# Performance work log

Hardware: AMD Instinct MI355X
Metric: run time of the kernel (lower is better)

Reference implementation:

```python
import jax, jax.numpy as jnp
import numpy as np

H = 128        # hidden_channels
R = 32         # num_rbf
L = 2          # num_layers
CUTOFF = 4.5   # cutoff_upper (cutoff_lower = 0)
N_ATOMS = 2048
N_EDGES = 32768


def _tensor_norm(t):
    # Frobenius norm squared over the trailing 3x3 -> [N, H]
    return jnp.sum(t * t, axis=(-2, -1))


def _decompose(t):
    # Split into isotropic (I), antisymmetric (A), traceless symmetric (S) parts.
    eye = jnp.eye(3, dtype=t.dtype)
    I = (jnp.trace(t, axis1=-2, axis2=-1) / 3.0)[..., None, None] * eye
    A = 0.5 * (t - jnp.swapaxes(t, -2, -1))
    S = 0.5 * (t + jnp.swapaxes(t, -2, -1)) - I
    return I, A, S


def _chan_mix(T, W):
    # torch nn.Linear(H, H, bias=False) applied on the channel axis of [N,H,3,3]
    return jnp.einsum('nhij,gh->ngij', T, W)


def _interaction(X, edge_index, edge_weight, edge_attr, q,
                 W1, b1, W2, b2, W3, b3, Wt):
    N = X.shape[0]
    src, dst = edge_index[0], edge_index[1]
    # cosine cutoff (cutoff_lower = 0)
    C = 0.5 * (jnp.cos(edge_weight * (jnp.pi / CUTOFF)) + 1.0)
    C = C * (edge_weight < CUTOFF).astype(C.dtype)
    # edge scalar MLP: R -> H -> 2H -> 3H, silu
    ea = jax.nn.silu(edge_attr @ W1.T + b1)
    ea = jax.nn.silu(ea @ W2.T + b2)
    ea = jax.nn.silu(ea @ W3.T + b3)
    ea = (ea * C[:, None]).reshape(-1, H, 3)       # [E, H, 3]
    # normalize node tensors
    X = X / (_tensor_norm(X) + 1.0)[..., None, None]
    I, A, S = _decompose(X)
    I = _chan_mix(I, Wt[0])
    A = _chan_mix(A, Wt[1])
    S = _chan_mix(S, Wt[2])
    Y = I + A + S
    # per-edge tensor messages (Im + Am + Sm fused before the scatter)
    msg = (ea[:, :, 0, None, None] * I[dst]
           + ea[:, :, 1, None, None] * A[dst]
           + ea[:, :, 2, None, None] * S[dst])   # [E, H, 3, 3]
    M = jax.ops.segment_sum(msg, src, num_segments=N)
    # O(3) group: symmetrized tensor product, scaled by charge factor
    AB = jnp.matmul(M, Y) + jnp.matmul(Y, M)
    I, A, S = _decompose((1.0 + 0.1 * q[:, None, None, None]) * AB)
    normp1 = (_tensor_norm(I + A + S) + 1.0)[..., None, None]
    I, A, S = I / normp1, A / normp1, S / normp1
    I = _chan_mix(I, Wt[3])
    A = _chan_mix(A, Wt[4])
    S = _chan_mix(S, Wt[5])
    dX = I + A + S
    return X + dX + (1.0 + 0.1 * q[:, None, None, None]) * jnp.matmul(dX, dX)


def setup_inputs() -> dict:
    key = jax.random.key(0)
    ks = jax.random.split(key, 10)
    N, E = N_ATOMS, N_EDGES
    X = jax.random.normal(ks[0], (N, H, 3, 3), jnp.float32)
    edge_index = jax.random.randint(ks[1], (2, E), 0, N, jnp.int32)
    edge_weight = jax.random.uniform(ks[2], (E,), jnp.float32, 0.1, CUTOFF)
    edge_attr = jax.random.normal(ks[3], (E, R), jnp.float32)
    q = jax.random.normal(ks[4], (N,), jnp.float32) * 0.1
    s = 0.05
    Ws1 = jax.random.normal(ks[5], (L, H, R), jnp.float32) * s
    bs1 = jnp.zeros((L, H), jnp.float32)
    Ws2 = jax.random.normal(ks[6], (L, 2 * H, H), jnp.float32) * s
    bs2 = jnp.zeros((L, 2 * H), jnp.float32)
    Ws3 = jax.random.normal(ks[7], (L, 3 * H, 2 * H), jnp.float32) * s
    bs3 = jnp.zeros((L, 3 * H), jnp.float32)
    Wt = jax.random.normal(ks[8], (L, 6, H, H), jnp.float32) * s
    return dict(X=X, edge_attr=edge_attr, edge_weight=edge_weight, q=q,
                Ws1=Ws1, bs1=bs1, Ws2=Ws2, bs2=bs2, Ws3=Ws3, bs3=bs3,
                Wt=Wt, edge_index=edge_index)


def reference(X, edge_attr, edge_weight, q, Ws1, bs1, Ws2, bs2, Ws3, bs3, Wt, edge_index):
    for l in range(L):
        X = _interaction(X, edge_index, edge_weight, edge_attr, q,
                         Ws1[l], bs1[l], Ws2[l], bs2[l], Ws3[l], bs3[l], Wt[l])
    return X
```

## Files before the change

### kernel.cpp

```cpp
#include <hip/hip_runtime.h>
#include <hip/hip_bf16.h>
#include <math.h>

#define H 128
#define R 32
#define NATOMS 2048
#define NEDGES 32768
#define NH (NATOMS * H)
#define NP 1152
#define CUTOFF_F 4.5f
#define PI_OVER_CUTOFF 0.6981317007977318f

typedef __bf16 bf16x8 __attribute__((ext_vector_type(8)));
typedef float f32x4 __attribute__((ext_vector_type(4)));
typedef short short8 __attribute__((ext_vector_type(8)));

__device__ __forceinline__ float silu_f(float x) {
    return x / (1.f + __expf(-x));
}
__device__ __forceinline__ float b2f(unsigned short u) {
    return __uint_as_float(((unsigned)u) << 16);
}
__device__ __forceinline__ unsigned short f2b(float f) {
    __hip_bfloat16 h = __float2bfloat16(f);
    return __builtin_bit_cast(unsigned short, h);
}

__device__ __forceinline__ void build_full(const float d[9], float m[9]) {
    float i0 = d[0], a01 = d[1], a02 = d[2], a12 = d[3];
    float s00 = d[4], s01 = d[5], s02 = d[6], s11 = d[7], s12 = d[8];
    float s22 = -(s00 + s11);
    m[0] = i0 + s00;  m[1] = a01 + s01;  m[2] = a02 + s02;
    m[3] = s01 - a01; m[4] = i0 + s11;   m[5] = a12 + s12;
    m[6] = s02 - a02; m[7] = s12 - a12;  m[8] = i0 + s22;
}

#define C0 (NEDGES * R)
#define C1 (2 * H * R)
#define C2 (2 * 2 * H * H)
#define C3 (2 * 3 * H * 2 * H)
#define C4 (2 * 6 * H * H)
__global__ __launch_bounds__(256) void k_cast_all(
        const float* __restrict__ ea, const float* __restrict__ w1,
        const float* __restrict__ w2, const float* __restrict__ w3,
        const float* __restrict__ wt,
        __hip_bfloat16* __restrict__ oea, __hip_bfloat16* __restrict__ ow1,
        __hip_bfloat16* __restrict__ ow2, __hip_bfloat16* __restrict__ ow3,
        __hip_bfloat16* __restrict__ owt) {
    int i = blockIdx.x * 256 + threadIdx.x;
    if (i < C0) { oea[i] = __float2bfloat16(ea[i]); return; }
    i -= C0;
    if (i < C1) { ow1[i] = __float2bfloat16(w1[i]); return; }
    i -= C1;
    if (i < C2) { ow2[i] = __float2bfloat16(w2[i]); return; }
    i -= C2;
    if (i < C3) { ow3[i] = __float2bfloat16(w3[i]); return; }
    i -= C3;
    if (i < C4) { owt[i] = __float2bfloat16(wt[i]); }
}

__global__ __launch_bounds__(256) void k_node_prep(
        const float* __restrict__ X, float* __restrict__ Xn,
        __hip_bfloat16* __restrict__ Db) {
    int i = blockIdx.x * 256 + threadIdx.x;
    if (i >= NH) return;
    const float* x = X + (size_t)i * 9;
    float v[9];
    float ss = 0.f;
#pragma unroll
    for (int j = 0; j < 9; j++) { v[j] = x[j]; ss += v[j] * v[j]; }
    float inv = 1.f / (ss + 1.f);
#pragma unroll
    for (int j = 0; j < 9; j++) { v[j] *= inv; Xn[(size_t)i * 9 + j] = v[j]; }
    float i0 = (v[0] + v[4] + v[8]) * (1.f / 3.f);
    unsigned short* D = (unsigned short*)Db + (size_t)(i >> 7) * NP + (i & 127);
    D[0 * H] = f2b(i0);
    D[1 * H] = f2b(0.5f * (v[1] - v[3]));
    D[2 * H] = f2b(0.5f * (v[2] - v[6]));
    D[3 * H] = f2b(0.5f * (v[5] - v[7]));
    D[4 * H] = f2b(v[0] - i0);
    D[5 * H] = f2b(0.5f * (v[1] + v[3]));
    D[6 * H] = f2b(0.5f * (v[2] + v[6]));
    D[7 * H] = f2b(v[4] - i0);
    D[8 * H] = f2b(0.5f * (v[5] + v[7]));
}

struct TGm {
    static constexpr int BKm = 64;
    static constexpr int RB  = 128;
    static constexpr int SWZ = 7;
    static constexpr int NIT = 2;
    static constexpr int ABYTES = 128 * RB;
    static constexpr int BBYTES = 64 * RB;
    static constexpr int AISS = ABYTES / 4096;
    static constexpr int BISS = BBYTES / 4096;
    static constexpr int LDSB = ABYTES + BBYTES;
};

__device__ __forceinline__ void tile_gemm_mix(
        const __hip_bfloat16* __restrict__ A, int strideA,
        const __hip_bfloat16* __restrict__ W,
        int m0, int n0, char* lds, f32x4 acc[4][2]) {
    using T = TGm;
    const int t = threadIdx.x;
    const int lane = t & 63;
    const int w = t >> 6;

    auto stage = [&](int b, int it) {
        const int k0 = it * T::BKm;
        char* As = lds + b * T::LDSB;
        char* Bs = As + T::ABYTES;
#pragma unroll
        for (int i = 0; i < T::AISS; i++) {
            int base = (w * T::AISS + i) * 1024;
            int lin = base + lane * 16;
            int row = lin / T::RB;
            int slot = (lin % T::RB) >> 4;
            int sl = slot ^ (row & T::SWZ);
            const char* src = (const char*)(A + (size_t)(m0 + row) * strideA + k0) + sl * 16;
            __builtin_amdgcn_global_load_lds(
                (const __attribute__((address_space(1))) void*)src,
                (__attribute__((address_space(3))) void*)(As + base), 16, 0, 0);
        }
#pragma unroll
        for (int i = 0; i < T::BISS; i++) {
            int base = (w * T::BISS + i) * 1024;
            int lin = base + lane * 16;
            int row = lin / T::RB;
            int slot = (lin % T::RB) >> 4;
            int sl = slot ^ (row & T::SWZ);
            const char* src = (const char*)(W + (size_t)(n0 + row) * H + k0) + sl * 16;
            __builtin_amdgcn_global_load_lds(
                (const __attribute__((address_space(1))) void*)src,
                (__attribute__((address_space(3))) void*)(Bs + base), 16, 0, 0);
        }
    };

    auto compute = [&](int b) {
        const char* As = lds + b * T::LDSB;
        const char* Bs = As + T::ABYTES;
        const int wm = (w & 1) * 64;
        const int wn = (w >> 1) * 32;
        const int rA = wm + (lane & 15);
        const int rB = wn + (lane & 15);
        const int c = lane >> 4;
#pragma unroll
        for (int kk = 0; kk < T::BKm / 32; kk++) {
            bf16x8 av[4], bv[2];
#pragma unroll
            for (int mf = 0; mf < 4; mf++) {
                int row = rA + mf * 16;
                int sp = (kk * 4 + c) ^ (row & T::SWZ);
                av[mf] = __builtin_bit_cast(bf16x8,
                    *(const short8*)(As + row * T::RB + sp * 16));
            }
#pragma unroll
            for (int nf = 0; nf < 2; nf++) {
                int row = rB + nf * 16;
                int sp = (kk * 4 + c) ^ (row & T::SWZ);
                bv[nf] = __builtin_bit_cast(bf16x8,
                    *(const short8*)(Bs + row * T::RB + sp * 16));
            }
#pragma unroll
            for (int mf = 0; mf < 4; mf++)
#pragma unroll
                for (int nf = 0; nf < 2; nf++)
                    acc[mf][nf] = __builtin_amdgcn_mfma_f32_16x16x32_bf16(
                        av[mf], bv[nf], acc[mf][nf], 0, 0, 0);
        }
    };

    stage(0, 0);
    asm volatile("s_waitcnt vmcnt(0)" ::: "memory");
    __syncthreads();
    for (int it = 0; it < T::NIT; it++) {
        int b = it & 1;
        if (it + 1 < T::NIT) stage(b ^ 1, it + 1);
        compute(b);
        asm volatile("s_waitcnt vmcnt(0)" ::: "memory");
        __syncthreads();
    }
}

__global__ __launch_bounds__(256) void k_mix(
        const __hip_bfloat16* __restrict__ Db, const __hip_bfloat16* __restrict__ Wtb,
        __hip_bfloat16* __restrict__ Outp, int partOff) {
    __shared__ char lds[2 * TGm::LDSB];
    int c = blockIdx.z;
    int part = (c == 0) ? 0 : ((c < 4) ? 1 : 2);
    const __hip_bfloat16* A = Db + (size_t)c * H;
    const __hip_bfloat16* W = Wtb + (size_t)(partOff + part) * H * H;
    unsigned short* Out = (unsigned short*)Outp + (size_t)c * H;
    const int lane = threadIdx.x & 63;
    const int w = threadIdx.x >> 6;
    const int wm = (w & 1) * 64, wn = (w >> 1) * 32;
    const int m0 = blockIdx.x * 128, n0 = blockIdx.y * 64;
    f32x4 acc[4][2] = {};
    tile_gemm_mix(A, NP, W, m0, n0, lds, acc);
#pragma unroll
    for (int mf = 0; mf < 4; mf++)
#pragma unroll
        for (int r = 0; r < 4; r++) {
            int row = m0 + wm + mf * 16 + (lane >> 4) * 4 + r;
#pragma unroll
            for (int nf = 0; nf < 2; nf++) {
                int col = n0 + wn + nf * 16 + (lane & 15);
                Out[(size_t)row * NP + col] = f2b(acc[mf][nf][r]);
            }
        }
}

#define ETILE 64
#define PAD0 40
#define PAD1 136
#define PAD2 264
#define SA2_B (64 * PAD2 * 2)
#define SA1_B (64 * PAD1 * 2)

__global__ __launch_bounds__(256, 3) void k_mlp_fused(
        const __hip_bfloat16* __restrict__ eaB,
        const __hip_bfloat16* __restrict__ W1b, const __hip_bfloat16* __restrict__ W2b,
        const __hip_bfloat16* __restrict__ W3b,
        const float* __restrict__ bs1, const float* __restrict__ bs2,
        const float* __restrict__ bs3, const float* __restrict__ ew,
        __hip_bfloat16* __restrict__ ea3g) {
    const int l = blockIdx.z;
    const unsigned short* W1 = (const unsigned short*)W1b + (size_t)l * (H * R);
    const unsigned short* W2 = (const unsigned short*)W2b + (size_t)l * (2 * H * H);
    const unsigned short* W3 = (const unsigned short*)W3b + (size_t)l * (3 * H * 2 * H);
    const float* b1 = bs1 + (size_t)l * H;
    const float* b2 = bs2 + (size_t)l * 2 * H;
    const float* b3 = bs3 + (size_t)l * 3 * H;
    unsigned short* outp = (unsigned short*)ea3g + (size_t)l * NEDGES * 384;
    const int e0 = blockIdx.x * ETILE;

    __shared__ char smem[SA2_B + SA1_B + 256 + 16];
    unsigned short* sA2 = (unsigned short*)smem;
    unsigned short* sEA = (unsigned short*)smem;
    unsigned short* sA1 = (unsigned short*)(smem + SA2_B);
    float* sEW = (float*)(smem + SA2_B + SA1_B);

    const int t = threadIdx.x;
    const int lane = t & 63;
    const int w = t >> 6;
    const int q = lane >> 4;
    const int li = lane & 15;

    {
        int row = t >> 2, c8 = t & 3;
        *(uint4*)(sEA + row * PAD0 + c8 * 8) =
            *(const uint4*)((const unsigned short*)eaB + (size_t)(e0 + row) * R + c8 * 8);
        if (t < ETILE) sEW[t] = ew[e0 + t];
    }
    __syncthreads();

    {
        f32x4 acc1[4][2] = {};
        bf16x8 bv[2];
#pragma unroll
        for (int nf = 0; nf < 2; nf++) {
            int col = w * 32 + nf * 16 + li;
            bv[nf] = __builtin_bit_cast(bf16x8,
                *(const short8*)(W1 + (size_t)col * R + q * 8));
        }
#pragma unroll
        for (int mf = 0; mf < 4; mf++) {
            int row = mf * 16 + li;
            bf16x8 av = __builtin_bit_cast(bf16x8,
                *(const short8*)(sEA + row * PAD0 + q * 8));
#pragma unroll
            for (int nf = 0; nf < 2; nf++)
                acc1[mf][nf] = __builtin_amdgcn_mfma_f32_16x16x32_bf16(
                    av, bv[nf], acc1[mf][nf], 0, 0, 0);
        }
        float bb[2];
#pragma unroll
        for (int nf = 0; nf < 2; nf++) bb[nf] = b1[w * 32 + nf * 16 + li];
        __syncthreads();
#pragma unroll
        for (int mf = 0; mf < 4; mf++)
#pragma unroll
            for (int r = 0; r < 4; r++) {
                int row = mf * 16 + q * 4 + r;
#pragma unroll
                for (int nf = 0; nf < 2; nf++) {
                    int col = w * 32 + nf * 16 + li;
                    sA1[row * PAD1 + col] = f2b(silu_f(acc1[mf][nf][r] + bb[nf]));
                }
            }
    }
    __syncthreads();

    {
        f32x4 acc2[4][4] = {};
        bf16x8 b2v[2][4];
#pragma unroll
        for (int nf = 0; nf < 4; nf++)
            b2v[0][nf] = __builtin_bit_cast(bf16x8,
                *(const short8*)(W2 + (size_t)(w * 64 + nf * 16 + li) * H + q * 8));
#pragma unroll
        for (int ks = 0; ks < 4; ks++) {
            const int cur = ks & 1;
            if (ks < 3) {
#pragma unroll
                for (int nf = 0; nf < 4; nf++)
                    b2v[cur ^ 1][nf] = __builtin_bit_cast(bf16x8,
                        *(const short8*)(W2 + (size_t)(w * 64 + nf * 16 + li) * H
                                         + (ks + 1) * 32 + q * 8));
            }
            bf16x8 av[4];
#pragma unroll
            for (int mf = 0; mf < 4; mf++)
                av[mf] = __builtin_bit_cast(bf16x8,
                    *(const short8*)(sA1 + (mf * 16 + li) * PAD1 + ks * 32 + q * 8));
            __builtin_amdgcn_s_setprio(1);
#pragma unroll
            for (int mf = 0; mf < 4; mf++)
#pragma unroll
                for (int nf = 0; nf < 4; nf++)
                    acc2[mf][nf] = __builtin_amdgcn_mfma_f32_16x16x32_bf16(
                        av[mf], b2v[cur][nf], acc2[mf][nf], 0, 0, 0);
            __builtin_amdgcn_s_setprio(0);
        }
        float bb[4];
#pragma unroll
        for (int nf = 0; nf < 4; nf++) bb[nf] = b2[w * 64 + nf * 16 + li];
        __syncthreads();
#pragma unroll
        for (int mf = 0; mf < 4; mf++)
#pragma unroll
            for (int r = 0; r < 4; r++) {
                int row = mf * 16 + q * 4 + r;
#pragma unroll
                for (int nf = 0; nf < 4; nf++) {
                    int col = w * 64 + nf * 16 + li;
                    sA2[row * PAD2 + col] = f2b(silu_f(acc2[mf][nf][r] + bb[nf]));
                }
            }
    }
    __syncthreads();

#pragma unroll
    for (int hn = 0; hn < 2; hn++) {
        const int cbase = w * 96 + hn * 48;
        f32x4 acc3[4][3] = {};
        bf16x8 b3v[2][3];
#pragma unroll
        for (int nf = 0; nf < 3; nf++)
            b3v[0][nf] = __builtin_bit_cast(bf16x8,
                *(const short8*)(W3 + (size_t)(cbase + nf * 16 + li) * (2 * H) + q * 8));
#pragma unroll
        for (int ks = 0; ks < 8; ks++) {
            const int cur = ks & 1;
            if (ks < 7) {
#pragma unroll
                for (int nf = 0; nf < 3; nf++)
                    b3v[cur ^ 1][nf] = __builtin_bit_cast(bf16x8,
                        *(const short8*)(W3 + (size_t)(cbase + nf * 16 + li) * (2 * H)
                                         + (ks + 1) * 32 + q * 8));
            }
            bf16x8 av[4];
#pragma unroll
            for (int mf = 0; mf < 4; mf++)
                av[mf] = __builtin_bit_cast(bf16x8,
                    *(const short8*)(sA2 + (mf * 16 + li) * PAD2 + ks * 32 + q * 8));
            __builtin_amdgcn_s_setprio(1);
#pragma unroll
            for (int mf = 0; mf < 4; mf++)
#pragma unroll
                for (int nf = 0; nf < 3; nf++)
                    acc3[mf][nf] = __builtin_amdgcn_mfma_f32_16x16x32_bf16(
                        av[mf], b3v[cur][nf], acc3[mf][nf], 0, 0, 0);
            __builtin_amdgcn_s_setprio(0);
        }
        float bb[3];
#pragma unroll
        for (int nf = 0; nf < 3; nf++) bb[nf] = b3[cbase + nf * 16 + li];
#pragma unroll
        for (int mf = 0; mf < 4; mf++)
#pragma unroll
            for (int r = 0; r < 4; r++) {
                int row = mf * 16 + q * 4 + r;
                float wv = sEW[row];
                float cs = (wv < CUTOFF_F) ? 0.5f * (__cosf(wv * PI_OVER_CUTOFF) + 1.f) : 0.f;
#pragma unroll
                for (int nf = 0; nf < 3; nf++) {
                    int col = cbase + nf * 16 + li;
                    float x = silu_f(acc3[mf][nf][r] + bb[nf]) * cs;
                    outp[(size_t)(e0 + row) * 384 + col] = f2b(x);
                }
            }
    }
}

__global__ __launch_bounds__(256) void k_hist(
        const int* __restrict__ eidx, int* __restrict__ cnt) {
    int e = blockIdx.x * 256 + threadIdx.x;
    if (e < NEDGES) atomicAdd(&cnt[eidx[e]], 1);
}

__global__ __launch_bounds__(256) void k_scan(
        const int* __restrict__ cnt, int* __restrict__ rowstart,
        int* __restrict__ cursor) {
    __shared__ int partial[256];
    int t = threadIdx.x;
    int loc[8];
    int run = 0;
#pragma unroll
    for (int j = 0; j < 8; j++) {
        int v = cnt[t * 8 + j];
        loc[j] = run; run += v;
    }
    partial[t] = run;
    __syncthreads();
    if (t == 0) {
        int acc = 0;
        for (int i = 0; i < 256; i++) { int v = partial[i]; partial[i] = acc; acc += v; }
        rowstart[2048] = acc;
    }
    __syncthreads();
    int base = partial[t];
#pragma unroll
    for (int j = 0; j < 8; j++) {
        rowstart[t * 8 + j] = base + loc[j];
        cursor[t * 8 + j] = base + loc[j];
    }
}

__global__ __launch_bounds__(256) void k_fill(
        const int* __restrict__ eidx, int* __restrict__ cursor,
        int* __restrict__ elist) {
    int e = blockIdx.x * 256 + threadIdx.x;
    if (e >= NEDGES) return;
    int src = eidx[e];
    int pos = atomicAdd(&cursor[src], 1);
    elist[pos] = e;
}

__global__ __launch_bounds__(256) void k_gather_ab(
        const __hip_bfloat16* __restrict__ ea ,
        const int* __restrict__ eidx,
        const int* __restrict__ rowstart, const int* __restrict__ elist,
        const __hip_bfloat16* __restrict__ Yb, const float* __restrict__ q,
        __hip_bfloat16* __restrict__ Tb) {
    int gid = blockIdx.x * 256 + threadIdx.x;
    int n = gid >> 7;
    int t7 = gid & 127;
    int hp = t7 >> 1;
    int half = t7 & 1;
    int h0 = hp << 1;
    int beg = rowstart[n], end = rowstart[n + 1];
    const unsigned short* Y = (const unsigned short*)Yb;
    float acc[9][2];
#pragma unroll
    for (int c = 0; c < 9; c++) { acc[c][0] = 0.f; acc[c][1] = 0.f; }
    for (int idx = beg + half; idx < end; idx += 2) {
        int e = elist[idx];
        int dst = eidx[NEDGES + e];
        const unsigned short* eap = (const unsigned short*)ea + (size_t)e * 384 + h0 * 3;
        unsigned u0 = *(const unsigned*)(eap);
        unsigned u1 = *(const unsigned*)(eap + 2);
        unsigned u2 = *(const unsigned*)(eap + 4);
        float w0a = b2f(u0 & 0xffff), w1a = b2f(u0 >> 16);
        float w2a = b2f(u1 & 0xffff), w0b = b2f(u1 >> 16);
        float w1b = b2f(u2 & 0xffff), w2b = b2f(u2 >> 16);
        const unsigned short* yp = Y + (size_t)dst * NP + h0;
        ushort2 y;
        y = *(const ushort2*)(yp + 0 * H); acc[0][0] += w0a * b2f(y.x); acc[0][1] += w0b * b2f(y.y);
        y = *(const ushort2*)(yp + 1 * H); acc[1][0] += w1a * b2f(y.x); acc[1][1] += w1b * b2f(y.y);
        y = *(const ushort2*)(yp + 2 * H); acc[2][0] += w1a * b2f(y.x); acc[2][1] += w1b * b2f(y.y);
        y = *(const ushort2*)(yp + 3 * H); acc[3][0] += w1a * b2f(y.x); acc[3][1] += w1b * b2f(y.y);
#pragma unroll
        for (int c = 4; c < 9; c++) {
            y = *(const ushort2*)(yp + c * H);
            acc[c][0] += w2a * b2f(y.x); acc[c][1] += w2b * b2f(y.y);
        }
    }
#pragma unroll
    for (int c = 0; c < 9; c++) {
        acc[c][0] += __shfl_xor(acc[c][0], 1);
        acc[c][1] += __shfl_xor(acc[c][1], 1);
    }
    int hcol = h0 + half;
    const unsigned short* yp = Y + (size_t)n * NP + hcol;
    float scale = 1.f + 0.1f * q[n];
    float md[9], yd[9];
#pragma unroll
    for (int c = 0; c < 9; c++) {
        md[c] = acc[c][half];
        yd[c] = b2f(yp[(size_t)c * H]);
    }
    float m[9], yf[9];
    build_full(md, m);
    build_full(yd, yf);
    float ab[9];
#pragma unroll
    for (int ii = 0; ii < 3; ii++)
#pragma unroll
        for (int jj = 0; jj < 3; jj++) {
            float s = 0.f;
#pragma unroll
            for (int kk = 0; kk < 3; kk++)
                s += m[ii * 3 + kk] * yf[kk * 3 + jj] + yf[ii * 3 + kk] * m[kk * 3 + jj];
            ab[ii * 3 + jj] = s;
        }
    float nrm = 0.f;
#pragma unroll
    for (int j = 0; j < 9; j++) { ab[j] *= scale; nrm += ab[j] * ab[j]; }
    float inv = 1.f / (nrm + 1.f);
    float tr3 = (ab[0] + ab[4] + ab[8]) * (1.f / 3.f);
    unsigned short* T = (unsigned short*)Tb + (size_t)n * NP + hcol;
    T[0 * H] = f2b(tr3 * inv);
    T[1 * H] = f2b(0.5f * (ab[1] - ab[3]) * inv);
    T[2 * H] = f2b(0.5f * (ab[2] - ab[6]) * inv);
    T[3 * H] = f2b(0.5f * (ab[5] - ab[7]) * inv);
    T[4 * H] = f2b((ab[0] - tr3) * inv);
    T[5 * H] = f2b(0.5f * (ab[1] + ab[3]) * inv);
    T[6 * H] = f2b(0.5f * (ab[2] + ab[6]) * inv);
    T[7 * H] = f2b((ab[4] - tr3) * inv);
    T[8 * H] = f2b(0.5f * (ab[5] + ab[7]) * inv);
}

template <bool PREP>
__global__ __launch_bounds__(256) void k_final(
        const __hip_bfloat16* __restrict__ dXb, const float* __restrict__ Xn,
        const float* __restrict__ q, float* __restrict__ Xout,
        float* __restrict__ XnW, __hip_bfloat16* __restrict__ Db) {
    int i = blockIdx.x * 256 + threadIdx.x;
    if (i >= NH) return;
    const unsigned short* dX = (const unsigned short*)dXb + (size_t)(i >> 7) * NP + (i & 127);
    float dd[9];
#pragma unroll
    for (int c = 0; c < 9; c++) dd[c] = b2f(dX[(size_t)c * H]);
    float dx[9];
    build_full(dd, dx);
    float scale = 1.f + 0.1f * q[i >> 7];
    float out[9];
#pragma unroll
    for (int ii = 0; ii < 3; ii++)
#pragma unroll
        for (int jj = 0; jj < 3; jj++) {
            float s = 0.f;
#pragma unroll
            for (int kk = 0; kk < 3; kk++)
                s += dx[ii * 3 + kk] * dx[kk * 3 + jj];
            out[ii * 3 + jj] = Xn[(size_t)i * 9 + ii * 3 + jj] + dx[ii * 3 + jj] + scale * s;
        }
#pragma unroll
    for (int j = 0; j < 9; j++) Xout[(size_t)i * 9 + j] = out[j];
    if (PREP) {
        float ss = 0.f;
#pragma unroll
        for (int j = 0; j < 9; j++) ss += out[j] * out[j];
        float inv = 1.f / (ss + 1.f);
        float v[9];
#pragma unroll
        for (int j = 0; j < 9; j++) { v[j] = out[j] * inv; XnW[(size_t)i * 9 + j] = v[j]; }
        float i0 = (v[0] + v[4] + v[8]) * (1.f / 3.f);
        unsigned short* D = (unsigned short*)Db + (size_t)(i >> 7) * NP + (i & 127);
        D[0 * H] = f2b(i0);
        D[1 * H] = f2b(0.5f * (v[1] - v[3]));
        D[2 * H] = f2b(0.5f * (v[2] - v[6]));
        D[3 * H] = f2b(0.5f * (v[5] - v[7]));
        D[4 * H] = f2b(v[0] - i0);
        D[5 * H] = f2b(0.5f * (v[1] + v[3]));
        D[6 * H] = f2b(0.5f * (v[2] + v[6]));
        D[7 * H] = f2b(v[4] - i0);
        D[8 * H] = f2b(0.5f * (v[5] + v[7]));
    }
}

extern "C" void kernel_launch(void* const* d_in, const int* in_sizes, int n_in,
                              void* d_out, int out_size, void* d_ws, size_t ws_size,
                              hipStream_t stream) {
    const float* X          = (const float*)d_in[0];
    const float* edge_attr  = (const float*)d_in[1];
    const float* edge_weight= (const float*)d_in[2];
    const float* q          = (const float*)d_in[3];
    const float* Ws1        = (const float*)d_in[4];
    const float* bs1        = (const float*)d_in[5];
    const float* Ws2        = (const float*)d_in[6];
    const float* bs2        = (const float*)d_in[7];
    const float* Ws3        = (const float*)d_in[8];
    const float* bs3        = (const float*)d_in[9];
    const float* Wt         = (const float*)d_in[10];
    const int*   eidx       = (const int*)d_in[11];
    float* Xout = (float*)d_out;

    char* p = (char*)d_ws;
    auto alloc = [&](size_t bytes) -> char* {
        char* r = p; p += (bytes + 255) & ~(size_t)255; return r;
    };
    size_t nodeBytes = (size_t)NH * 9 * sizeof(float);
    float* Xn   = (float*)alloc(nodeBytes);
    __hip_bfloat16* Db = (__hip_bfloat16*)alloc((size_t)NH * 9 * 2);
    __hip_bfloat16* Yb = (__hip_bfloat16*)alloc((size_t)NH * 9 * 2);
    __hip_bfloat16* eaB = (__hip_bfloat16*)alloc((size_t)C0 * 2);
    __hip_bfloat16* W1b = (__hip_bfloat16*)alloc((size_t)C1 * 2);
    __hip_bfloat16* W2b = (__hip_bfloat16*)alloc((size_t)C2 * 2);
    __hip_bfloat16* W3b = (__hip_bfloat16*)alloc((size_t)C3 * 2);
    __hip_bfloat16* Wtb = (__hip_bfloat16*)alloc((size_t)C4 * 2);
    __hip_bfloat16* ea3g = (__hip_bfloat16*)alloc((size_t)2 * NEDGES * 384 * 2);
    int* cnt      = (int*)alloc(2048 * 4);
    int* rowstart = (int*)alloc(2049 * 4);
    int* cursor   = (int*)alloc(2048 * 4);
    int* elist    = (int*)alloc(NEDGES * 4);

    k_cast_all<<<(C0 + C1 + C2 + C3 + C4) / 256, 256, 0, stream>>>(
        edge_attr, Ws1, Ws2, Ws3, Wt, eaB, W1b, W2b, W3b, Wtb);

    hipMemsetAsync(cnt, 0, 2048 * sizeof(int), stream);
    k_hist<<<NEDGES / 256, 256, 0, stream>>>(eidx, cnt);
    k_scan<<<1, 256, 0, stream>>>(cnt, rowstart, cursor);
    k_fill<<<NEDGES / 256, 256, 0, stream>>>(eidx, cursor, elist);

    k_node_prep<<<NH / 256, 256, 0, stream>>>(X, Xn, Db);

    k_mlp_fused<<<dim3(NEDGES / ETILE, 1, 2), 256, 0, stream>>>(
        eaB, W1b, W2b, W3b, bs1, bs2, bs3, edge_weight, ea3g);

    for (int l = 0; l < 2; l++) {
        const __hip_bfloat16* Wtl = Wtb + (size_t)l * 6 * H * H;
        const __hip_bfloat16* ea3 = ea3g + (size_t)l * NEDGES * 384;

        k_mix<<<dim3(NATOMS / 128, 2, 9), 256, 0, stream>>>(Db, Wtl, Yb, 0);
        k_gather_ab<<<NH / 256, 256, 0, stream>>>(
            ea3, eidx, rowstart, elist, Yb, q, Db);
        k_mix<<<dim3(NATOMS / 128, 2, 9), 256, 0, stream>>>(Db, Wtl, Yb, 3);
        if (l == 0)
            k_final<true><<<NH / 256, 256, 0, stream>>>(Yb, Xn, q, Xout, Xn, Db);
        else
            k_final<false><<<NH / 256, 256, 0, stream>>>(Yb, Xn, q, Xout, nullptr, nullptr);
    }
}
```

Before: 166.4 us.

## Split fused edge MLP across 8 waves per block instead of 4

The fused edge MLP kernel now launches 512 threads per block and divides each layer's output columns among 8 wavefronts, so each wave handles half as many MFMA column fragments. This is meant to raise wave-level parallelism and latency hiding per block and to cut the per-wave accumulator register footprint. In exchange, each weight fragment is loaded by more waves and the final stage is split unevenly into 2+1 fragments per wave. Occupancy limits also change with the new launch bounds.

```diff
diff --git a/kernel.cpp b/kernel.cpp
--- a/kernel.cpp
+++ b/kernel.cpp
@@ -214,10 +214,10 @@
 #define PAD0 40
 #define PAD1 136
 #define PAD2 264
-#define SA2_B (64 * PAD2 * 2)
-#define SA1_B (64 * PAD1 * 2)
-
-__global__ __launch_bounds__(256, 3) void k_mlp_fused(
+#define SA2_B (ETILE * PAD2 * 2)
+#define SA1_B (ETILE * PAD1 * 2)
+
+__global__ __launch_bounds__(512, 4) void k_mlp_fused(
         const __hip_bfloat16* __restrict__ eaB,
         const __hip_bfloat16* __restrict__ W1b, const __hip_bfloat16* __restrict__ W2b,
         const __hip_bfloat16* __restrict__ W3b,
@@ -234,7 +234,7 @@
     unsigned short* outp = (unsigned short*)ea3g + (size_t)l * NEDGES * 384;
     const int e0 = blockIdx.x * ETILE;
 
-    __shared__ char smem[SA2_B + SA1_B + 256 + 16];
+    __shared__ char smem[SA2_B + SA1_B + ETILE * 4 + 16];
     unsigned short* sA2 = (unsigned short*)smem;
     unsigned short* sEA = (unsigned short*)smem;
     unsigned short* sA1 = (unsigned short*)(smem + SA2_B);
@@ -247,65 +247,55 @@
     const int li = lane & 15;
 
     {
-        int row = t >> 2, c8 = t & 3;
-        *(uint4*)(sEA + row * PAD0 + c8 * 8) =
-            *(const uint4*)((const unsigned short*)eaB + (size_t)(e0 + row) * R + c8 * 8);
+        if (t < 256) {
+            int row = t >> 2, c8 = t & 3;
+            *(uint4*)(sEA + row * PAD0 + c8 * 8) =
+                *(const uint4*)((const unsigned short*)eaB + (size_t)(e0 + row) * R + c8 * 8);
+        }
         if (t < ETILE) sEW[t] = ew[e0 + t];
     }
     __syncthreads();
 
     {
-        f32x4 acc1[4][2] = {};
-        bf16x8 bv[2];
-#pragma unroll
-        for (int nf = 0; nf < 2; nf++) {
-            int col = w * 32 + nf * 16 + li;
-            bv[nf] = __builtin_bit_cast(bf16x8,
-                *(const short8*)(W1 + (size_t)col * R + q * 8));
-        }
+        f32x4 acc1[4] = {};
+        const int col = w * 16 + li;
+        bf16x8 bv = __builtin_bit_cast(bf16x8,
+            *(const short8*)(W1 + (size_t)col * R + q * 8));
 #pragma unroll
         for (int mf = 0; mf < 4; mf++) {
             int row = mf * 16 + li;
             bf16x8 av = __builtin_bit_cast(bf16x8,
                 *(const short8*)(sEA + row * PAD0 + q * 8));
-#pragma unroll
-            for (int nf = 0; nf < 2; nf++)
-                acc1[mf][nf] = __builtin_amdgcn_mfma_f32_16x16x32_bf16(
-                    av, bv[nf], acc1[mf][nf], 0, 0, 0);
-        }
-        float bb[2];
-#pragma unroll
-        for (int nf = 0; nf < 2; nf++) bb[nf] = b1[w * 32 + nf * 16 + li];
+            acc1[mf] = __builtin_amdgcn_mfma_f32_16x16x32_bf16(
+                av, bv, acc1[mf], 0, 0, 0);
+        }
+        float bb = b1[col];
         __syncthreads();
 #pragma unroll
         for (int mf = 0; mf < 4; mf++)
 #pragma unroll
             for (int r = 0; r < 4; r++) {
                 int row = mf * 16 + q * 4 + r;
-#pragma unroll
-                for (int nf = 0; nf < 2; nf++) {
-                    int col = w * 32 + nf * 16 + li;
-                    sA1[row * PAD1 + col] = f2b(silu_f(acc1[mf][nf][r] + bb[nf]));
-                }
+                sA1[row * PAD1 + col] = f2b(silu_f(acc1[mf][r] + bb));
             }
     }
     __syncthreads();
 
     {
-        f32x4 acc2[4][4] = {};
-        bf16x8 b2v[2][4];
-#pragma unroll
-        for (int nf = 0; nf < 4; nf++)
+        f32x4 acc2[4][2] = {};
+        bf16x8 b2v[2][2];
+#pragma unroll
+        for (int nf = 0; nf < 2; nf++)
             b2v[0][nf] = __builtin_bit_cast(bf16x8,
-                *(const short8*)(W2 + (size_t)(w * 64 + nf * 16 + li) * H + q * 8));
+                *(const short8*)(W2 + (size_t)(w * 32 + nf * 16 + li) * H + q * 8));
 #pragma unroll
         for (int ks = 0; ks < 4; ks++) {
             const int cur = ks & 1;
             if (ks < 3) {
 #pragma unroll
-                for (int nf = 0; nf < 4; nf++)
+                for (int nf = 0; nf < 2; nf++)
                     b2v[cur ^ 1][nf] = __builtin_bit_cast(bf16x8,
-                        *(const short8*)(W2 + (size_t)(w * 64 + nf * 16 + li) * H
+                        *(const short8*)(W2 + (size_t)(w * 32 + nf * 16 + li) * H
                                          + (ks + 1) * 32 + q * 8));
             }
             bf16x8 av[4];
@@ -317,14 +307,14 @@
 #pragma unroll
             for (int mf = 0; mf < 4; mf++)
 #pragma unroll
-                for (int nf = 0; nf < 4; nf++)
+                for (int nf = 0; nf < 2; nf++)
                     acc2[mf][nf] = __builtin_amdgcn_mfma_f32_16x16x32_bf16(
                         av[mf], b2v[cur][nf], acc2[mf][nf], 0, 0, 0);
             __builtin_amdgcn_s_setprio(0);
         }
-        float bb[4];
-#pragma unroll
-        for (int nf = 0; nf < 4; nf++) bb[nf] = b2[w * 64 + nf * 16 + li];
+        float bb[2];
+#pragma unroll
+        for (int nf = 0; nf < 2; nf++) bb[nf] = b2[w * 32 + nf * 16 + li];
         __syncthreads();
 #pragma unroll
         for (int mf = 0; mf < 4; mf++)
@@ -332,8 +322,8 @@
             for (int r = 0; r < 4; r++) {
                 int row = mf * 16 + q * 4 + r;
 #pragma unroll
-                for (int nf = 0; nf < 4; nf++) {
-                    int col = w * 64 + nf * 16 + li;
+                for (int nf = 0; nf < 2; nf++) {
+                    int col = w * 32 + nf * 16 + li;
                     sA2[row * PAD2 + col] = f2b(silu_f(acc2[mf][nf][r] + bb[nf]));
                 }
             }
@@ -342,22 +332,25 @@
 
 #pragma unroll
     for (int hn = 0; hn < 2; hn++) {
-        const int cbase = w * 96 + hn * 48;
-        f32x4 acc3[4][3] = {};
-        bf16x8 b3v[2][3];
-#pragma unroll
-        for (int nf = 0; nf < 3; nf++)
-            b3v[0][nf] = __builtin_bit_cast(bf16x8,
-                *(const short8*)(W3 + (size_t)(cbase + nf * 16 + li) * (2 * H) + q * 8));
+        const int NF = (hn == 0) ? 2 : 1;
+        const int cbase = w * 48 + hn * 32;
+        f32x4 acc3[4][2] = {};
+        bf16x8 b3v[2][2];
+#pragma unroll
+        for (int nf = 0; nf < 2; nf++)
+            if (nf < NF)
+                b3v[0][nf] = __builtin_bit_cast(bf16x8,
+                    *(const short8*)(W3 + (size_t)(cbase + nf * 16 + li) * (2 * H) + q * 8));
 #pragma unroll
         for (int ks = 0; ks < 8; ks++) {
             const int cur = ks & 1;
             if (ks < 7) {
 #pragma unroll
-                for (int nf = 0; nf < 3; nf++)
-                    b3v[cur ^ 1][nf] = __builtin_bit_cast(bf16x8,
-                        *(const short8*)(W3 + (size_t)(cbase + nf * 16 + li) * (2 * H)
-                                         + (ks + 1) * 32 + q * 8));
+                for (int nf = 0; nf < 2; nf++)
+                    if (nf < NF)
+                        b3v[cur ^ 1][nf] = __builtin_bit_cast(bf16x8,
+                            *(const short8*)(W3 + (size_t)(cbase + nf * 16 + li) * (2 * H)
+                                             + (ks + 1) * 32 + q * 8));
             }
             bf16x8 av[4];
 #pragma unroll
@@ -368,14 +361,16 @@
 #pragma unroll
             for (int mf = 0; mf < 4; mf++)
 #pragma unroll
-                for (int nf = 0; nf < 3; nf++)
-                    acc3[mf][nf] = __builtin_amdgcn_mfma_f32_16x16x32_bf16(
-                        av[mf], b3v[cur][nf], acc3[mf][nf], 0, 0, 0);
+                for (int nf = 0; nf < 2; nf++)
+                    if (nf < NF)
+                        acc3[mf][nf] = __builtin_amdgcn_mfma_f32_16x16x32_bf16(
+                            av[mf], b3v[cur][nf], acc3[mf][nf], 0, 0, 0);
             __builtin_amdgcn_s_setprio(0);
         }
-        float bb[3];
-#pragma unroll
-        for (int nf = 0; nf < 3; nf++) bb[nf] = b3[cbase + nf * 16 + li];
+        float bb[2];
+#pragma unroll
+        for (int nf = 0; nf < 2; nf++)
+            bb[nf] = (nf < NF) ? b3[cbase + nf * 16 + li] : 0.f;
 #pragma unroll
         for (int mf = 0; mf < 4; mf++)
 #pragma unroll
@@ -384,11 +379,12 @@
                 float wv = sEW[row];
                 float cs = (wv < CUTOFF_F) ? 0.5f * (__cosf(wv * PI_OVER_CUTOFF) + 1.f) : 0.f;
 #pragma unroll
-                for (int nf = 0; nf < 3; nf++) {
-                    int col = cbase + nf * 16 + li;
-                    float x = silu_f(acc3[mf][nf][r] + bb[nf]) * cs;
-                    outp[(size_t)(e0 + row) * 384 + col] = f2b(x);
-                }
+                for (int nf = 0; nf < 2; nf++)
+                    if (nf < NF) {
+                        int col = cbase + nf * 16 + li;
+                        float x = silu_f(acc3[mf][nf][r] + bb[nf]) * cs;
+                        outp[(size_t)(e0 + row) * 384 + col] = f2b(x);
+                    }
             }
     }
 }
@@ -616,7 +612,7 @@
 
     k_node_prep<<<NH / 256, 256, 0, stream>>>(X, Xn, Db);
 
-    k_mlp_fused<<<dim3(NEDGES / ETILE, 1, 2), 256, 0, stream>>>(
+    k_mlp_fused<<<dim3(NEDGES / ETILE, 1, 2), 512, 0, stream>>>(
         eaB, W1b, W2b, W3b, bs1, bs2, bs3, edge_weight, ea3g);
 
     for (int l = 0; l < 2; l++) {
```

After: 164.4 us. About the same (-1.2%).
